# Kernel tuning notes

Measured on AMD Instinct MI355X. Metric: run time of the kernel, lower is better.

## Reference

```python
import jax, jax.numpy as jnp
import numpy as np

B, T, C = 2, 2048, 2048
H, Hk, D = 32, 4, 64
N_REP = H // Hk
THETA = 10000.0


def _rope_tables():
    inv_freq = 1.0 / (THETA ** (np.arange(0, D, 2, dtype=np.float64) / D))  # [D/2]
    t = np.arange(T, dtype=np.float64)
    freqs = np.outer(t, inv_freq)                # [T, D/2]
    emb = np.repeat(freqs, 2, axis=-1)           # interleaved [T, D]
    return jnp.asarray(np.cos(emb), jnp.float32), jnp.asarray(np.sin(emb), jnp.float32)


def setup_inputs() -> dict:
    key = jax.random.key(0)
    kx, kq, kk, kv, ko = jax.random.split(key, 5)
    scale = 0.02
    x = jax.random.normal(kx, (B, T, C), jnp.float32)
    wq = jax.random.normal(kq, (H * D, C), jnp.float32) * scale
    wk = jax.random.normal(kk, (Hk * D, C), jnp.float32) * scale
    wv = jax.random.normal(kv, (Hk * D, C), jnp.float32) * scale
    wo = jax.random.normal(ko, (C, H * D), jnp.float32) * scale
    cos, sin = _rope_tables()
    return {"x": x, "cos": cos, "sin": sin, "wq": wq, "wk": wk, "wv": wv, "wo": wo}


def _apply_rope(x, cos, sin):
    # x: [B, h, T, D]; cos/sin: [T, D] interleaved
    x1 = x[..., 0::2]
    x2 = x[..., 1::2]
    rot = jnp.stack([-x2, x1], axis=-1).reshape(x.shape)
    return x * cos[None, None] + rot * sin[None, None]


def reference(x, cos, sin, wq, wk, wv, wo):
    q = (x @ wq.T).reshape(B, T, H, D).transpose(0, 2, 1, 3)    # [B,H,T,D]
    k = (x @ wk.T).reshape(B, T, Hk, D).transpose(0, 2, 1, 3)   # [B,Hk,T,D]
    v = (x @ wv.T).reshape(B, T, Hk, D).transpose(0, 2, 1, 3)   # [B,Hk,T,D]
    q = _apply_rope(q, cos, sin)
    k = _apply_rope(k, cos, sin)
    # new_cache = (k, v) pre-repeat
    kr = jnp.repeat(k, N_REP, axis=1)                            # [B,H,T,D]
    vr = jnp.repeat(v, N_REP, axis=1)
    scores = jnp.einsum('bhtd,bhsd->bhts', q, kr) / jnp.sqrt(jnp.float32(D))
    mask = jnp.tril(jnp.ones((T, T), dtype=bool))                # causal (kv_cache is None)
    scores = jnp.where(mask, scores, jnp.finfo(scores.dtype).min)
    attn = jax.nn.softmax(scores, axis=-1)
    o = jnp.einsum('bhts,bhsd->bhtd', attn, vr)
    o = o.transpose(0, 2, 1, 3).reshape(B, T, H * D)
    return (o @ wo.T, k, v)
```

## Files before the change

### kernel.cpp

```cpp
#include <hip/hip_runtime.h>
#include <hip/hip_bf16.h>

#define B_ 2
#define T_ 2048
#define C_ 2048
#define H_ 32
#define HK_ 4
#define D_ 64

typedef __attribute__((ext_vector_type(4)))  float f32x4;
typedef __attribute__((ext_vector_type(2)))  float f32x2;
typedef __attribute__((ext_vector_type(16))) float f32x16;
typedef __attribute__((ext_vector_type(8)))  short bf16x8;

static __device__ __forceinline__ unsigned short f2bf(float f) {
  union { __hip_bfloat16 h; unsigned short s; } u;
  u.h = __float2bfloat16(f);
  return u.s;
}
static __device__ __forceinline__ float bf2f(unsigned short s) {
  union { unsigned int u; float f; } u; u.u = ((unsigned int)s) << 16; return u.f;
}
static __device__ __forceinline__ unsigned int cvtpk(float lo, float hi) {
  unsigned int r;
  asm("v_cvt_pk_bf16_f32 %0, %1, %2" : "=v"(r) : "v"(lo), "v"(hi));
  return r;
}

#define GLD16(gp, lp) __builtin_amdgcn_global_load_lds( \
    (const __attribute__((address_space(1))) unsigned int*)(gp), \
    (__attribute__((address_space(3))) unsigned int*)(unsigned int)(uintptr_t)(lp), 16, 0, 0)

__global__ void conv_all(const float* __restrict__ x,  const float* __restrict__ wq,
                         const float* __restrict__ wk, const float* __restrict__ wv,
                         const float* __restrict__ wo,
                         unsigned short* __restrict__ x_bf,
                         unsigned short* __restrict__ wqkv,
                         unsigned short* __restrict__ wo_bf) {
  const int i = blockIdx.x * blockDim.x + threadIdx.x;
  const float* src;
  unsigned short* dst;
  int off;
  if (i < 2097152)      { src = x;  dst = x_bf;                  off = i; }
  else if (i < 3145728) { src = wq; dst = wqkv;                  off = i - 2097152; }
  else if (i < 3276800) { src = wk; dst = wqkv + 2048 * 2048;    off = i - 3145728; }
  else if (i < 3407872) { src = wv; dst = wqkv + 2304 * 2048;    off = i - 3276800; }
  else                  { src = wo; dst = wo_bf;                 off = i - 3407872; }
  f32x4 v = *(const f32x4*)(src + 4 * (size_t)off);
  ushort4 o;
  o.x = f2bf(v[0]); o.y = f2bf(v[1]); o.z = f2bf(v[2]); o.w = f2bf(v[3]);
  *(ushort4*)(dst + 4 * (size_t)off) = o;
}

template<int EPI>
__global__ __launch_bounds__(256, 3)
void gemm3(const unsigned short* __restrict__ A, const unsigned short* __restrict__ W,
           int M, int N, int K,
           float* __restrict__ Cf,
           const float* __restrict__ cosT, const float* __restrict__ sinT,
           unsigned short* __restrict__ qb, unsigned short* __restrict__ kbf,
           unsigned short* __restrict__ vtb, float* __restrict__ koutf,
           float* __restrict__ voutf) {
  __shared__ unsigned short As[3][128 * 32];
  __shared__ unsigned short Ws[3][128 * 32];

  const int tid  = threadIdx.x;
  const int lane = tid & 63;
  const int w    = tid >> 6;
  const int wm   = w >> 1, wn = w & 1;
  const int g    = lane >> 4;
  const int lr   = lane & 15;

  const int gx   = gridDim.x;
  const int flat = blockIdx.y * gx + blockIdx.x;
  const int cpx  = (gx * gridDim.y) >> 3;
  const int swzb = (flat & 7) * cpx + (flat >> 3);
  const int bm   = (swzb / gx) * 128;
  const int bn   = (swzb % gx) * 128;

  const int srow = tid >> 2;
  const int sc   = (tid & 3) ^ (srow & 3);
  const unsigned short* Ag = A + (size_t)(bm + srow) * K + sc * 8;
  const unsigned short* Wg = W + (size_t)(bn + srow) * K + sc * 8;

#define STAGE3(buf, k0) do { \
    GLD16(Ag + (k0),                  &As[buf][       w * 512]); \
    GLD16(Ag + (size_t)64 * K + (k0), &As[buf][2048 + w * 512]); \
    GLD16(Wg + (k0),                  &Ws[buf][       w * 512]); \
    GLD16(Wg + (size_t)64 * K + (k0), &Ws[buf][2048 + w * 512]); \
  } while (0)

  f32x4 acc[4][4] = {};

  const int nt = K >> 5;
  STAGE3(0, 0);
  STAGE3(1, 32);

  for (int t = 0; t < nt; ++t) {
    if (t + 1 < nt) asm volatile("s_waitcnt vmcnt(4)" ::: "memory");
    else            asm volatile("s_waitcnt vmcnt(0)" ::: "memory");
    asm volatile("s_barrier" ::: "memory");

    if (t + 2 < nt) {
      const int nb = (t + 2) % 3;
      STAGE3(nb, (size_t)(t + 2) * 32);
    }

    const unsigned short* At = &As[t % 3][0];
    const unsigned short* Wt = &Ws[t % 3][0];

    bf16x8 af[4], wf[4];
#pragma unroll
    for (int m = 0; m < 4; m++) {
      const int row = wm * 64 + m * 16 + lr;
      af[m] = *(const bf16x8*)&At[row * 32 + ((g ^ (row & 3)) << 3)];
    }
#pragma unroll
    for (int n = 0; n < 4; n++) {
      const int row = wn * 64 + n * 16 + lr;
      wf[n] = *(const bf16x8*)&Wt[row * 32 + ((g ^ (row & 3)) << 3)];
    }
    __builtin_amdgcn_s_setprio(1);
#pragma unroll
    for (int m = 0; m < 4; m++)
#pragma unroll
      for (int n = 0; n < 4; n++)
        acc[m][n] = __builtin_amdgcn_mfma_f32_16x16x32_bf16(af[m], wf[n], acc[m][n], 0, 0, 0);
    __builtin_amdgcn_s_setprio(0);
  }
#undef STAGE3

  if (EPI == 0) {
#pragma unroll
    for (int m = 0; m < 4; m++) {
      const int row = bm + wm * 64 + m * 16 + g * 4;
#pragma unroll
      for (int n = 0; n < 4; n++) {
        const int col = bn + wn * 64 + n * 16 + lr;
#pragma unroll
        for (int r = 0; r < 4; r++)
          Cf[(size_t)(row + r) * N + col] = acc[m][n][r];
      }
    }
  } else {
    const int seg = (bn < 2048) ? 0 : (bn < 2304 ? 1 : 2);
#pragma unroll
    for (int m = 0; m < 4; m++) {
#pragma unroll
      for (int n = 0; n < 4; n++) {
        const int col = bn + wn * 64 + n * 16 + lr;
        const int d   = col & 63;
#pragma unroll
        for (int r = 0; r < 4; r++) {
          const int row = bm + wm * 64 + m * 16 + g * 4 + r;
          const int tt  = row & (T_ - 1);
          const int bb  = row >> 11;
          const float val = acc[m][n][r];
          if (seg == 2) {
            const int hk = (col >> 6) - 36;
            const size_t idx = ((size_t)(bb * HK_ + hk) * T_ + tt) * D_ + d;
            voutf[idx] = val;
            const int tm   = tt & 15;
            const int tpos = (tt & ~15) | ((tm & 3) + ((tm >> 3) << 2) + ((tm & 4) << 1));
            vtb[((size_t)(bb * HK_ + hk) * D_ + d) * T_ + tpos] = f2bf(val);
          } else {
            const float cs = cosT[tt * D_ + d];
            const float sn = sinT[tt * D_ + d];
            const float other = __shfl_xor(val, 1);
            const float o = val * cs + ((lr & 1) ? other : -other) * sn;
            if (seg == 0) {
              const int h = col >> 6;
              qb[((size_t)(bb * H_ + h) * T_ + tt) * D_ + d] = f2bf(o);
            } else {
              const int hk = (col >> 6) - 32;
              const size_t idx = ((size_t)(bb * HK_ + hk) * T_ + tt) * D_ + d;
              koutf[idx] = o;
              kbf[idx]   = f2bf(o);
            }
          }
        }
      }
    }
  }
}

__global__ __launch_bounds__(512, 4)
void gqa_attn4(const unsigned short* __restrict__ qb,
               const unsigned short* __restrict__ kb,
               const unsigned short* __restrict__ vt,
               unsigned short* __restrict__ ob) {
  __shared__ unsigned short Ks[3][4096];
  __shared__ unsigned short Vs[3][4096];

  const int tid  = threadIdx.x;
  const int lane = tid & 63;
  const int w    = tid >> 6;
  const int qi   = lane & 31;
  const int hi   = lane >> 5;

  const int qt = 63 - (int)(blockIdx.x >> 3);
  const int go = blockIdx.x & 7;
  const int b  = go >> 2;
  const int hk = go & 3;
  const int h  = hk * 8 + w;
  const int bh = b * H_ + h;

  const int qbase = qt * 32;
  const int qrow  = qbase + qi;

  const unsigned short* qptr = qb + ((size_t)bh * T_ + qrow) * D_ + 8 * hi;
  bf16x8 qf[4];
#pragma unroll
  for (int c = 0; c < 4; c++) qf[c] = *(const bf16x8*)(qptr + 16 * c);

  const int srow   = lane >> 3;
  const int schunk = (lane & 7) ^ srow;
  const int krow   = 8 * w + srow;
  const unsigned short* gK = kb + (size_t)(b * HK_ + hk) * T_ * D_ + (size_t)krow * D_ + schunk * 8;
  const unsigned short* gV = vt + (size_t)(b * HK_ + hk) * D_ * T_ + (size_t)krow * T_ + schunk * 8;
  unsigned short* ldsK = &Ks[0][w * 512];
  unsigned short* ldsV = &Vs[0][w * 512];

#define STAGE_KV(pp, kk0) do { \
    GLD16(gK + (size_t)(kk0) * D_, ldsK + (pp) * 4096); \
    GLD16(gV + (kk0),              ldsV + (pp) * 4096); \
  } while (0)

  f32x16 o0 = {}, o1 = {};
  float m = -1e30f, l = 0.f;
  float c1 = 0.f;
  const float SC   = 0.125f * 1.44269504089f;
  const float THRR = 44.3614195f;
  const int   swz  = qi & 7;

  const int nt = ((qbase + 31) >> 6) + 1;
  STAGE_KV(0, 0);
  if (nt > 1) STAGE_KV(1, 64);

  int p = 0;
  for (int it = 0; it < nt; ++it) {
    const int kb0 = it * 64;
    const bool last = (it == nt - 1);
    const bool has1 = (kb0 + 32 <= qbase + 31);

    asm volatile("s_waitcnt lgkmcnt(0)" ::: "memory");
    if (it + 1 < nt) asm volatile("s_waitcnt vmcnt(2)" ::: "memory");
    else             asm volatile("s_waitcnt vmcnt(0)" ::: "memory");
    asm volatile("s_barrier" ::: "memory");
    if (it + 2 < nt) STAGE_KV((p + 2 > 2) ? p - 1 : p + 2, kb0 + 128);

    const unsigned short* Kt = &Ks[0][0] + p * 4096;
    const unsigned short* Vt = &Vs[0][0] + p * 4096;

    f32x16 st0 = {}, st1 = {};
    __builtin_amdgcn_s_setprio(1);
#pragma unroll
    for (int c = 0; c < 4; c++) {
      bf16x8 kf = *(const bf16x8*)&Kt[qi * 64 + (((hi + 2 * c) ^ swz) << 3)];
      st0 = __builtin_amdgcn_mfma_f32_32x32x16_bf16(kf, qf[c], st0, 0, 0, 0);
    }
    if (!last || has1) {
#pragma unroll
      for (int c = 0; c < 4; c++) {
        bf16x8 kf = *(const bf16x8*)&Kt[(32 + qi) * 64 + (((hi + 2 * c) ^ swz) << 3)];
        st1 = __builtin_amdgcn_mfma_f32_32x32x16_bf16(kf, qf[c], st1, 0, 0, 0);
      }
    }
    __builtin_amdgcn_s_setprio(0);

    if (last) {
#pragma unroll
      for (int r = 0; r < 16; ++r) {
        const int key = kb0 + (r & 3) + 8 * (r >> 2) + 4 * hi;
        st0[r] = (key      <= qrow) ? st0[r] : -1e30f;
        st1[r] = (key + 32 <= qrow) ? st1[r] : -1e30f;
      }
    }

    float tmax = fmaxf(st0[0], st0[1]);
#pragma unroll
    for (int r = 2; r < 16; ++r) tmax = fmaxf(tmax, st0[r]);
#pragma unroll
    for (int r = 0; r < 16; ++r) tmax = fmaxf(tmax, st1[r]);
    tmax = fmaxf(tmax, __shfl_xor(tmax, 32));

    if (!__all(tmax <= m + THRR)) {
      const float mnew  = fmaxf(m, tmax);
      const float al    = __builtin_amdgcn_exp2f((m - mnew) * SC);
#pragma unroll
      for (int r = 0; r < 16; ++r) { o0[r] *= al; o1[r] *= al; }
      l *= al;
      m  = mnew;
      c1 = -m * SC;
    }

    float sum = 0.f;
#pragma unroll
    for (int r = 0; r < 16; ++r) { float pv = __builtin_amdgcn_exp2f(__builtin_fmaf(st0[r], SC, c1)); st0[r] = pv; sum += pv; }
#pragma unroll
    for (int r = 0; r < 16; ++r) { float pv = __builtin_amdgcn_exp2f(__builtin_fmaf(st1[r], SC, c1)); st1[r] = pv; sum += pv; }
    sum += __shfl_xor(sum, 32);
    l += sum;

    union U8 { bf16x8 v; unsigned int u[4]; };
    U8 pf[4];
#pragma unroll
    for (int j = 0; j < 4; ++j) {
      pf[0].u[j] = cvtpk(st0[2 * j],     st0[2 * j + 1]);
      pf[1].u[j] = cvtpk(st0[8 + 2 * j], st0[8 + 2 * j + 1]);
      pf[2].u[j] = cvtpk(st1[2 * j],     st1[2 * j + 1]);
      pf[3].u[j] = cvtpk(st1[8 + 2 * j], st1[8 + 2 * j + 1]);
    }

    const int ncf = (!last || has1) ? 4 : 2;
    __builtin_amdgcn_s_setprio(1);
#pragma unroll
    for (int dh = 0; dh < 2; ++dh) {
      const unsigned short* Vrow = &Vt[(dh * 32 + qi) * 64];
      f32x16 oc = dh ? o1 : o0;
#pragma unroll
      for (int c = 0; c < 4; ++c) {
        if (c >= ncf) break;
        bf16x8 vf = *(const bf16x8*)&Vrow[(((2 * c + hi) ^ swz) << 3)];
        oc = __builtin_amdgcn_mfma_f32_32x32x16_bf16(vf, pf[c].v, oc, 0, 0, 0);
      }
      if (dh) o1 = oc; else o0 = oc;
    }
    __builtin_amdgcn_s_setprio(0);

    p = (p > 1) ? 0 : p + 1;
  }

  const float inv = 1.0f / l;
  unsigned short* orow = ob + (size_t)(b * T_ + qrow) * (H_ * D_) + h * D_;
#pragma unroll
  for (int dh = 0; dh < 2; ++dh) {
    const f32x16 ov = dh ? o1 : o0;
#pragma unroll
    for (int rg = 0; rg < 4; ++rg) {
      const int d0 = 32 * dh + 8 * rg + 4 * hi;
      ushort4 pk;
      pk.x = f2bf(ov[4 * rg + 0] * inv);
      pk.y = f2bf(ov[4 * rg + 1] * inv);
      pk.z = f2bf(ov[4 * rg + 2] * inv);
      pk.w = f2bf(ov[4 * rg + 3] * inv);
      *(ushort4*)(orow + d0) = pk;
    }
  }
#undef STAGE_KV
}

extern "C" void kernel_launch(void* const* d_in, const int* in_sizes, int n_in,
                              void* d_out, int out_size, void* d_ws, size_t ws_size,
                              hipStream_t stream) {
  const float* x    = (const float*)d_in[0];
  const float* cosT = (const float*)d_in[1];
  const float* sinT = (const float*)d_in[2];
  const float* wq   = (const float*)d_in[3];
  const float* wk   = (const float*)d_in[4];
  const float* wv   = (const float*)d_in[5];
  const float* wo   = (const float*)d_in[6];

  float* y    = (float*)d_out;
  float* kout = (float*)d_out + (size_t)B_ * T_ * C_;
  float* vout = kout + (size_t)B_ * HK_ * T_ * D_;

  char* ws = (char*)d_ws;
  unsigned short* x_bf = (unsigned short*)(ws);
  unsigned short* o_bf = x_bf;
  unsigned short* wqkv = (unsigned short*)(ws + 16777216);
  unsigned short* q_bf = (unsigned short*)(ws + 27262976);
  unsigned short* k_bf = (unsigned short*)(ws + 44040192);
  unsigned short* v_t  = (unsigned short*)(ws + 46137344);
  unsigned short* wo_bf= (unsigned short*)(ws + 48234496);

  const int M = B_ * T_;

  conv_all<<<17408, 256, 0, stream>>>(x, wq, wk, wv, wo, x_bf, wqkv, wo_bf);

  gemm3<1><<<dim3(2560 / 128, M / 128), 256, 0, stream>>>(
      x_bf, wqkv, M, 2560, C_, nullptr, cosT, sinT, q_bf, k_bf, v_t, kout, vout);

  gqa_attn4<<<512, 512, 0, stream>>>(q_bf, k_bf, v_t, o_bf);

  gemm3<0><<<dim3(C_ / 128, M / 128), 256, 0, stream>>>(
      o_bf, wo_bf, M, C_, H_ * D_, y, nullptr, nullptr, nullptr, nullptr, nullptr, nullptr, nullptr);
}
```

Baseline: 190.4 us.

## Pair complementary causal query tiles per block to balance work and reuse KV

Each attention block now handles two 32-row query tiles, one near the end of the sequence and one near the start, so every block does about the same amount of causal work. Each KV tile staged in shared memory is used by both query tiles, which halves KV loads per query and halves the grid to 256 blocks. The cost is doubled accumulator register state, with launch bounds lowered from 4 to 2 waves per SIMD, so occupancy drops. The fewer, larger blocks may also fill the GPU's compute units less well.

```diff
diff --git a/kernel.cpp b/kernel.cpp
--- a/kernel.cpp
+++ b/kernel.cpp
@@ -184,8 +184,96 @@
   }
 }
 
-__global__ __launch_bounds__(512, 4)
-void gqa_attn4(const unsigned short* __restrict__ qb,
+static __device__ __forceinline__ void attn_qstep(
+    const unsigned short* __restrict__ Kt, const unsigned short* __restrict__ Vt,
+    const bf16x8 (&qf)[4], f32x16& o0, f32x16& o1,
+    float& m, float& l, float& c1,
+    const int qrow, const int kb0, const bool last,
+    const int qi, const int hi, const int swz) {
+  const float SC   = 0.125f * 1.44269504089f;
+  const float THRR = 44.3614195f;
+  const int  qtop  = (qrow & ~31) + 31;
+  const bool has1  = (kb0 + 32 <= qtop);
+
+  f32x16 st0 = {}, st1 = {};
+  __builtin_amdgcn_s_setprio(1);
+#pragma unroll
+  for (int c = 0; c < 4; c++) {
+    bf16x8 kf = *(const bf16x8*)&Kt[qi * 64 + (((hi + 2 * c) ^ swz) << 3)];
+    st0 = __builtin_amdgcn_mfma_f32_32x32x16_bf16(kf, qf[c], st0, 0, 0, 0);
+  }
+  if (!last || has1) {
+#pragma unroll
+    for (int c = 0; c < 4; c++) {
+      bf16x8 kf = *(const bf16x8*)&Kt[(32 + qi) * 64 + (((hi + 2 * c) ^ swz) << 3)];
+      st1 = __builtin_amdgcn_mfma_f32_32x32x16_bf16(kf, qf[c], st1, 0, 0, 0);
+    }
+  }
+  __builtin_amdgcn_s_setprio(0);
+
+  if (last) {
+#pragma unroll
+    for (int r = 0; r < 16; ++r) {
+      const int key = kb0 + (r & 3) + 8 * (r >> 2) + 4 * hi;
+      st0[r] = (key      <= qrow) ? st0[r] : -1e30f;
+      st1[r] = (key + 32 <= qrow) ? st1[r] : -1e30f;
+    }
+  }
+
+  float tmax = fmaxf(st0[0], st0[1]);
+#pragma unroll
+  for (int r = 2; r < 16; ++r) tmax = fmaxf(tmax, st0[r]);
+#pragma unroll
+  for (int r = 0; r < 16; ++r) tmax = fmaxf(tmax, st1[r]);
+  tmax = fmaxf(tmax, __shfl_xor(tmax, 32));
+
+  if (!__all(tmax <= m + THRR)) {
+    const float mnew = fmaxf(m, tmax);
+    const float al   = __builtin_amdgcn_exp2f((m - mnew) * SC);
+#pragma unroll
+    for (int r = 0; r < 16; ++r) { o0[r] *= al; o1[r] *= al; }
+    l *= al;
+    m  = mnew;
+    c1 = -m * SC;
+  }
+
+  float sum = 0.f;
+#pragma unroll
+  for (int r = 0; r < 16; ++r) { float pv = __builtin_amdgcn_exp2f(__builtin_fmaf(st0[r], SC, c1)); st0[r] = pv; sum += pv; }
+#pragma unroll
+  for (int r = 0; r < 16; ++r) { float pv = __builtin_amdgcn_exp2f(__builtin_fmaf(st1[r], SC, c1)); st1[r] = pv; sum += pv; }
+  sum += __shfl_xor(sum, 32);
+  l += sum;
+
+  union U8 { bf16x8 v; unsigned int u[4]; };
+  U8 pf[4];
+#pragma unroll
+  for (int j = 0; j < 4; ++j) {
+    pf[0].u[j] = cvtpk(st0[2 * j],     st0[2 * j + 1]);
+    pf[1].u[j] = cvtpk(st0[8 + 2 * j], st0[8 + 2 * j + 1]);
+    pf[2].u[j] = cvtpk(st1[2 * j],     st1[2 * j + 1]);
+    pf[3].u[j] = cvtpk(st1[8 + 2 * j], st1[8 + 2 * j + 1]);
+  }
+
+  const int ncf = (!last || has1) ? 4 : 2;
+  __builtin_amdgcn_s_setprio(1);
+#pragma unroll
+  for (int dh = 0; dh < 2; ++dh) {
+    const unsigned short* Vrow = &Vt[(dh * 32 + qi) * 64];
+    f32x16 oc = dh ? o1 : o0;
+#pragma unroll
+    for (int c = 0; c < 4; ++c) {
+      if (c >= ncf) break;
+      bf16x8 vf = *(const bf16x8*)&Vrow[(((2 * c + hi) ^ swz) << 3)];
+      oc = __builtin_amdgcn_mfma_f32_32x32x16_bf16(vf, pf[c].v, oc, 0, 0, 0);
+    }
+    if (dh) o1 = oc; else o0 = oc;
+  }
+  __builtin_amdgcn_s_setprio(0);
+}
+
+__global__ __launch_bounds__(512, 2)
+void gqa_attn5(const unsigned short* __restrict__ qb,
                const unsigned short* __restrict__ kb,
                const unsigned short* __restrict__ vt,
                unsigned short* __restrict__ ob) {
@@ -198,20 +286,28 @@
   const int qi   = lane & 31;
   const int hi   = lane >> 5;
 
-  const int qt = 63 - (int)(blockIdx.x >> 3);
   const int go = blockIdx.x & 7;
+  const int pp = blockIdx.x >> 3;
   const int b  = go >> 2;
   const int hk = go & 3;
   const int h  = hk * 8 + w;
   const int bh = b * H_ + h;
 
-  const int qbase = qt * 32;
-  const int qrow  = qbase + qi;
-
-  const unsigned short* qptr = qb + ((size_t)bh * T_ + qrow) * D_ + 8 * hi;
-  bf16x8 qf[4];
-#pragma unroll
-  for (int c = 0; c < 4; c++) qf[c] = *(const bf16x8*)(qptr + 16 * c);
+  const int qbaseA = (63 - pp) * 32;
+  const int qbaseB = pp * 32;
+  const int qrowA  = qbaseA + qi;
+  const int qrowB  = qbaseB + qi;
+
+  bf16x8 qfA[4], qfB[4];
+  {
+    const unsigned short* qpA = qb + ((size_t)bh * T_ + qrowA) * D_ + 8 * hi;
+    const unsigned short* qpB = qb + ((size_t)bh * T_ + qrowB) * D_ + 8 * hi;
+#pragma unroll
+    for (int c = 0; c < 4; c++) {
+      qfA[c] = *(const bf16x8*)(qpA + 16 * c);
+      qfB[c] = *(const bf16x8*)(qpB + 16 * c);
+    }
+  }
 
   const int srow   = lane >> 3;
   const int schunk = (lane & 7) ^ srow;
@@ -221,130 +317,64 @@
   unsigned short* ldsK = &Ks[0][w * 512];
   unsigned short* ldsV = &Vs[0][w * 512];
 
-#define STAGE_KV(pp, kk0) do { \
-    GLD16(gK + (size_t)(kk0) * D_, ldsK + (pp) * 4096); \
-    GLD16(gV + (kk0),              ldsV + (pp) * 4096); \
+#define STAGE_KV(pbuf, kk0) do { \
+    GLD16(gK + (size_t)(kk0) * D_, ldsK + (pbuf) * 4096); \
+    GLD16(gV + (kk0),              ldsV + (pbuf) * 4096); \
   } while (0)
 
-  f32x16 o0 = {}, o1 = {};
-  float m = -1e30f, l = 0.f;
-  float c1 = 0.f;
-  const float SC   = 0.125f * 1.44269504089f;
-  const float THRR = 44.3614195f;
-  const int   swz  = qi & 7;
-
-  const int nt = ((qbase + 31) >> 6) + 1;
+  f32x16 o0A = {}, o1A = {}, o0B = {}, o1B = {};
+  float mA = -1e30f, lA = 0.f, c1A = 0.f;
+  float mB = -1e30f, lB = 0.f, c1B = 0.f;
+  const int swz = qi & 7;
+
+  const int ntA = ((qbaseA + 31) >> 6) + 1;
+  const int ntB = ((qbaseB + 31) >> 6) + 1;
+
   STAGE_KV(0, 0);
-  if (nt > 1) STAGE_KV(1, 64);
+  if (ntA > 1) STAGE_KV(1, 64);
 
   int p = 0;
-  for (int it = 0; it < nt; ++it) {
+  for (int it = 0; it < ntA; ++it) {
     const int kb0 = it * 64;
-    const bool last = (it == nt - 1);
-    const bool has1 = (kb0 + 32 <= qbase + 31);
 
     asm volatile("s_waitcnt lgkmcnt(0)" ::: "memory");
-    if (it + 1 < nt) asm volatile("s_waitcnt vmcnt(2)" ::: "memory");
-    else             asm volatile("s_waitcnt vmcnt(0)" ::: "memory");
+    if (it + 1 < ntA) asm volatile("s_waitcnt vmcnt(2)" ::: "memory");
+    else              asm volatile("s_waitcnt vmcnt(0)" ::: "memory");
     asm volatile("s_barrier" ::: "memory");
-    if (it + 2 < nt) STAGE_KV((p + 2 > 2) ? p - 1 : p + 2, kb0 + 128);
+    if (it + 2 < ntA) STAGE_KV((p + 2 > 2) ? p - 1 : p + 2, kb0 + 128);
 
     const unsigned short* Kt = &Ks[0][0] + p * 4096;
     const unsigned short* Vt = &Vs[0][0] + p * 4096;
 
-    f32x16 st0 = {}, st1 = {};
-    __builtin_amdgcn_s_setprio(1);
-#pragma unroll
-    for (int c = 0; c < 4; c++) {
-      bf16x8 kf = *(const bf16x8*)&Kt[qi * 64 + (((hi + 2 * c) ^ swz) << 3)];
-      st0 = __builtin_amdgcn_mfma_f32_32x32x16_bf16(kf, qf[c], st0, 0, 0, 0);
-    }
-    if (!last || has1) {
-#pragma unroll
-      for (int c = 0; c < 4; c++) {
-        bf16x8 kf = *(const bf16x8*)&Kt[(32 + qi) * 64 + (((hi + 2 * c) ^ swz) << 3)];
-        st1 = __builtin_amdgcn_mfma_f32_32x32x16_bf16(kf, qf[c], st1, 0, 0, 0);
-      }
-    }
-    __builtin_amdgcn_s_setprio(0);
-
-    if (last) {
-#pragma unroll
-      for (int r = 0; r < 16; ++r) {
-        const int key = kb0 + (r & 3) + 8 * (r >> 2) + 4 * hi;
-        st0[r] = (key      <= qrow) ? st0[r] : -1e30f;
-        st1[r] = (key + 32 <= qrow) ? st1[r] : -1e30f;
-      }
-    }
-
-    float tmax = fmaxf(st0[0], st0[1]);
-#pragma unroll
-    for (int r = 2; r < 16; ++r) tmax = fmaxf(tmax, st0[r]);
-#pragma unroll
-    for (int r = 0; r < 16; ++r) tmax = fmaxf(tmax, st1[r]);
-    tmax = fmaxf(tmax, __shfl_xor(tmax, 32));
-
-    if (!__all(tmax <= m + THRR)) {
-      const float mnew  = fmaxf(m, tmax);
-      const float al    = __builtin_amdgcn_exp2f((m - mnew) * SC);
-#pragma unroll
-      for (int r = 0; r < 16; ++r) { o0[r] *= al; o1[r] *= al; }
-      l *= al;
-      m  = mnew;
-      c1 = -m * SC;
-    }
-
-    float sum = 0.f;
-#pragma unroll
-    for (int r = 0; r < 16; ++r) { float pv = __builtin_amdgcn_exp2f(__builtin_fmaf(st0[r], SC, c1)); st0[r] = pv; sum += pv; }
-#pragma unroll
-    for (int r = 0; r < 16; ++r) { float pv = __builtin_amdgcn_exp2f(__builtin_fmaf(st1[r], SC, c1)); st1[r] = pv; sum += pv; }
-    sum += __shfl_xor(sum, 32);
-    l += sum;
-
-    union U8 { bf16x8 v; unsigned int u[4]; };
-    U8 pf[4];
-#pragma unroll
-    for (int j = 0; j < 4; ++j) {
-      pf[0].u[j] = cvtpk(st0[2 * j],     st0[2 * j + 1]);
-      pf[1].u[j] = cvtpk(st0[8 + 2 * j], st0[8 + 2 * j + 1]);
-      pf[2].u[j] = cvtpk(st1[2 * j],     st1[2 * j + 1]);
-      pf[3].u[j] = cvtpk(st1[8 + 2 * j], st1[8 + 2 * j + 1]);
-    }
-
-    const int ncf = (!last || has1) ? 4 : 2;
-    __builtin_amdgcn_s_setprio(1);
-#pragma unroll
-    for (int dh = 0; dh < 2; ++dh) {
-      const unsigned short* Vrow = &Vt[(dh * 32 + qi) * 64];
-      f32x16 oc = dh ? o1 : o0;
-#pragma unroll
-      for (int c = 0; c < 4; ++c) {
-        if (c >= ncf) break;
-        bf16x8 vf = *(const bf16x8*)&Vrow[(((2 * c + hi) ^ swz) << 3)];
-        oc = __builtin_amdgcn_mfma_f32_32x32x16_bf16(vf, pf[c].v, oc, 0, 0, 0);
-      }
-      if (dh) o1 = oc; else o0 = oc;
-    }
-    __builtin_amdgcn_s_setprio(0);
+    attn_qstep(Kt, Vt, qfA, o0A, o1A, mA, lA, c1A, qrowA, kb0, it == ntA - 1, qi, hi, swz);
+    if (it < ntB)
+      attn_qstep(Kt, Vt, qfB, o0B, o1B, mB, lB, c1B, qrowB, kb0, it == ntB - 1, qi, hi, swz);
 
     p = (p > 1) ? 0 : p + 1;
   }
 
-  const float inv = 1.0f / l;
-  unsigned short* orow = ob + (size_t)(b * T_ + qrow) * (H_ * D_) + h * D_;
+  const float invA = 1.0f / lA;
+  const float invB = 1.0f / lB;
+  unsigned short* orowA = ob + (size_t)(b * T_ + qrowA) * (H_ * D_) + h * D_;
+  unsigned short* orowB = ob + (size_t)(b * T_ + qrowB) * (H_ * D_) + h * D_;
 #pragma unroll
   for (int dh = 0; dh < 2; ++dh) {
-    const f32x16 ov = dh ? o1 : o0;
+    const f32x16 ovA = dh ? o1A : o0A;
+    const f32x16 ovB = dh ? o1B : o0B;
 #pragma unroll
     for (int rg = 0; rg < 4; ++rg) {
       const int d0 = 32 * dh + 8 * rg + 4 * hi;
-      ushort4 pk;
-      pk.x = f2bf(ov[4 * rg + 0] * inv);
-      pk.y = f2bf(ov[4 * rg + 1] * inv);
-      pk.z = f2bf(ov[4 * rg + 2] * inv);
-      pk.w = f2bf(ov[4 * rg + 3] * inv);
-      *(ushort4*)(orow + d0) = pk;
+      ushort4 pkA, pkB;
+      pkA.x = f2bf(ovA[4 * rg + 0] * invA);
+      pkA.y = f2bf(ovA[4 * rg + 1] * invA);
+      pkA.z = f2bf(ovA[4 * rg + 2] * invA);
+      pkA.w = f2bf(ovA[4 * rg + 3] * invA);
+      pkB.x = f2bf(ovB[4 * rg + 0] * invB);
+      pkB.y = f2bf(ovB[4 * rg + 1] * invB);
+      pkB.z = f2bf(ovB[4 * rg + 2] * invB);
+      pkB.w = f2bf(ovB[4 * rg + 3] * invB);
+      *(ushort4*)(orowA + d0) = pkA;
+      *(ushort4*)(orowB + d0) = pkB;
     }
   }
 #undef STAGE_KV
@@ -381,7 +411,7 @@
   gemm3<1><<<dim3(2560 / 128, M / 128), 256, 0, stream>>>(
       x_bf, wqkv, M, 2560, C_, nullptr, cosT, sinT, q_bf, k_bf, v_t, kout, vout);
 
-  gqa_attn4<<<512, 512, 0, stream>>>(q_bf, k_bf, v_t, o_bf);
+  gqa_attn5<<<256, 512, 0, stream>>>(q_bf, k_bf, v_t, o_bf);
 
   gemm3<0><<<dim3(C_ / 128, M / 128), 256, 0, stream>>>(
       o_bf, wo_bf, M, C_, H_ * D_, y, nullptr, nullptr, nullptr, nullptr, nullptr, nullptr, nullptr);
```

New measurement: 187.0 us, median of 3. No clear change (-1.8%).
